# Optimization experiments

Measured on AMD Instinct MI355X. Metric: run time of the kernel, lower is better.

Reference implementation:

```python
import jax, jax.numpy as jnp
import numpy as np

T, B, D, H, O = 128, 256, 512, 1024, 1


def setup_inputs() -> dict:
    key = jax.random.key(0)
    ks = jax.random.split(key, 10)
    s_in = 1.0 / np.sqrt(D)
    s_h = 1.0 / np.sqrt(H)
    u = lambda k, shape, s: jax.random.uniform(k, shape, jnp.float32, -s, s)
    return {
        "inputs": jax.random.normal(ks[0], (T, B, D), jnp.float32),
        "hidden_state": jnp.zeros((1, B, H), jnp.float32),
        "cell_state": jnp.zeros((1, B, H), jnp.float32),
        "W1": u(ks[1], (H, D), s_in),
        "b1": u(ks[2], (H,), s_in),
        "W_ih": u(ks[3], (4 * H, H), s_h),
        "W_hh": u(ks[4], (4 * H, H), s_h),
        "b_ih": u(ks[5], (4 * H,), s_h),
        "b_hh": u(ks[6], (4 * H,), s_h),
        "W_out": u(ks[7], (O, H), s_h),
        "b_out": u(ks[8], (O,), s_h),
    }


def reference(inputs, hidden_state, cell_state, W1, b1, W_ih, W_hh, b_ih, b_hh, W_out, b_out):
    # first_layer + ReLU (dropout is identity in eval mode)
    x = jax.nn.relu(jnp.einsum("tbd,hd->tbh", inputs, W1) + b1)  # (T,B,H)
    # Precompute input contribution to all gates for every timestep.
    xg = jnp.einsum("tbh,gh->tbg", x, W_ih) + b_ih + b_hh  # (T,B,4H)
    h0 = hidden_state[0]
    c0 = cell_state[0]

    def step(carry, xg_t):
        h, c = carry
        g = xg_t + h @ W_hh.T  # (B,4H), PyTorch gate order i,f,g,o
        i, f, gg, o = jnp.split(g, 4, axis=-1)
        i = jax.nn.sigmoid(i)
        f = jax.nn.sigmoid(f)
        gg = jnp.tanh(gg)
        o = jax.nn.sigmoid(o)
        c = f * c + i * gg
        h = o * jnp.tanh(c)
        return (h, c), h

    (hT, cT), hs = jax.lax.scan(step, (h0, c0), xg)
    out = jnp.einsum("tbh,oh->tbo", hs, W_out) + b_out  # (T,B,O)
    return out, hT[None], cT[None]
```

## Files before the change

### kernel.cpp

```cpp
#include <hip/hip_runtime.h>
#include <hip/hip_bf16.h>
#include <math.h>


#define T_STEPS 128
#define BATCH   256
#define DIM     512
#define HID     1024
#define GATES   4096
#define FPAD    32

typedef __attribute__((ext_vector_type(8))) short short8;
typedef __attribute__((ext_vector_type(4))) float f4;
typedef __attribute__((ext_vector_type(4))) int i4;

__device__ __forceinline__ short f2bf(float f) {
    union { float f; unsigned u; } x; x.f = f;
    unsigned r = (x.u + 0x7fffu + ((x.u >> 16) & 1u)) >> 16;
    return (short)r;
}
__device__ __forceinline__ float bf2f(short s) {
    union { unsigned u; float f; } x; x.u = ((unsigned)(unsigned short)s) << 16;
    return x.f;
}
__device__ __forceinline__ float sigm(float x) { return 1.f / (1.f + __expf(-x)); }
__device__ __forceinline__ float tanh_fast(float x) { return 2.f / (1.f + __expf(-2.f * x)) - 1.f; }

__device__ __forceinline__ void gll16(const void* g, void* l) {
    __builtin_amdgcn_global_load_lds(
        (const __attribute__((address_space(1))) void*)g,
        (__attribute__((address_space(3))) void*)l, 16, 0, 0);
}
__device__ __forceinline__ void store16_wt(void* p, i4 v) {
    asm volatile("global_store_dwordx4 %0, %1, off sc0 sc1"
                 :: "v"(p), "v"(v) : "memory");
}

__global__ __launch_bounds__(256) void cvt_f32_bf16(const float* __restrict__ in,
                                                    short* __restrict__ out, int n4) {
    int i = blockIdx.x * 256 + threadIdx.x;
    if (i < n4) {
        float4 v = ((const float4*)in)[i];
        union { short s[4]; long long ll; } r;
        r.s[0] = f2bf(v.x); r.s[1] = f2bf(v.y); r.s[2] = f2bf(v.z); r.s[3] = f2bf(v.w);
        ((long long*)out)[i] = r.ll;
    }
}

__global__ __launch_bounds__(256) void cvt_h0_blocked(const float* __restrict__ h0,
                                                      short* __restrict__ dst) {
    int b = blockIdx.x, k0 = threadIdx.x * 4;
    float4 v = *(const float4*)&h0[(size_t)b * HID + k0];
    union { short s[4]; long long ll; } p;
    p.s[0] = f2bf(v.x); p.s[1] = f2bf(v.y); p.s[2] = f2bf(v.z); p.s[3] = f2bf(v.w);
    *(long long*)&dst[(k0 >> 3) * (BATCH * 8) + b * 8 + (k0 & 7)] = p.ll;
}

__global__ __launch_bounds__(256) void cvt_permute_rows(const float* __restrict__ in,
                                                        short* __restrict__ out) {
    int r = blockIdx.x;
    int hc = r >> 2, g = r & 3;
    const float* src = in + (size_t)(g * HID + hc) * HID;
    short* dst = out + (size_t)r * HID;
    int c = threadIdx.x * 4;
    float4 v = *(const float4*)&src[c];
    union { short s[4]; long long ll; } p;
    p.s[0] = f2bf(v.x); p.s[1] = f2bf(v.y); p.s[2] = f2bf(v.z); p.s[3] = f2bf(v.w);
    *(long long*)&dst[c] = p.ll;
}

__global__ __launch_bounds__(256) void bias_sum_perm(const float* __restrict__ a,
                                                     const float* __restrict__ b,
                                                     float* __restrict__ o) {
    int r = blockIdx.x * 256 + threadIdx.x;
    int hc = r >> 2, g = r & 3;
    int src = g * HID + hc;
    o[r] = a[src] + b[src];
}

__global__ __launch_bounds__(256) void copy_f32v4(const float* __restrict__ in,
                                                  float* __restrict__ out, int n4) {
    int i = blockIdx.x * 256 + threadIdx.x;
    if (i < n4) ((float4*)out)[i] = ((const float4*)in)[i];
}

__global__ __launch_bounds__(256) void zero_i32(int* __restrict__ p, int n) {
    for (int i = blockIdx.x * 256 + threadIdx.x; i < n; i += gridDim.x * 256)
        p[i] = 0;
}

__global__ __launch_bounds__(256) void gemm_bt2(const short* __restrict__ A,
                                                const short* __restrict__ B,
                                                const float* __restrict__ bias,
                                                short* __restrict__ C,
                                                int M, int N, int K, int do_relu) {
    __shared__ __align__(16) short As[2][128 * 64];
    __shared__ __align__(16) short Bs[2][128 * 64];
    const int tid = threadIdx.x, wave = tid >> 6, lane = tid & 63;
    const int wm = (wave >> 1) * 64, wn = (wave & 1) * 64;

    const int nwg = gridDim.x * gridDim.y;
    const int flat = blockIdx.y * gridDim.x + blockIdx.x;
    const int qq = nwg >> 3, rr = nwg & 7;
    const int xcd = flat & 7, oin = flat >> 3;
    const int swz = (xcd < rr ? xcd * (qq + 1) : rr * (qq + 1) + (xcd - rr) * qq) + oin;
    const int bm = (swz % gridDim.x) * 128, bn = (swz / gridDim.x) * 128;

#define STAGE2(bufi, kt)                                                       \
    {                                                                          \
        const int k0_ = (kt) * 64;                                             \
        _Pragma("unroll")                                                      \
        for (int u = 0; u < 4; ++u) {                                          \
            int r0 = wave * 32 + u * 8;                                        \
            int row = r0 + (lane >> 3);                                        \
            int kof = ((lane & 7) ^ (row & 7)) * 8;                            \
            gll16(&A[(size_t)(bm + row) * K + k0_ + kof], &As[bufi][r0 * 64]); \
            gll16(&B[(size_t)(bn + row) * K + k0_ + kof], &Bs[bufi][r0 * 64]); \
        }                                                                      \
    }

    f4 acc[4][4] = {};
    const int NT = K >> 6;

    STAGE2(0, 0)
    __syncthreads();

    int cur = 0;
    for (int kt = 0; kt < NT; ++kt) {
        if (kt + 1 < NT) STAGE2(cur ^ 1, kt + 1)

#pragma unroll
        for (int ks = 0; ks < 2; ++ks) {
            short8 af[4], bfr[4];
#pragma unroll
            for (int i = 0; i < 4; ++i) {
                int ra = wm + i * 16 + (lane & 15);
                int sa = (ks * 4 + (lane >> 4)) ^ (ra & 7);
                af[i] = *(const short8*)&As[cur][ra * 64 + sa * 8];
                int rb = wn + i * 16 + (lane & 15);
                int sb = (ks * 4 + (lane >> 4)) ^ (rb & 7);
                bfr[i] = *(const short8*)&Bs[cur][rb * 64 + sb * 8];
            }
            __builtin_amdgcn_s_setprio(1);
#pragma unroll
            for (int i = 0; i < 4; ++i)
#pragma unroll
                for (int j = 0; j < 4; ++j)
                    acc[i][j] = __builtin_amdgcn_mfma_f32_16x16x32_bf16(af[i], bfr[j], acc[i][j], 0, 0, 0);
            __builtin_amdgcn_s_setprio(0);
        }
        __syncthreads();
        cur ^= 1;
    }
#undef STAGE2

    const int lc = lane & 15, lr = (lane >> 4) * 4;
#pragma unroll
    for (int i = 0; i < 4; ++i) {
#pragma unroll
        for (int j = 0; j < 4; ++j) {
            int col = bn + wn + j * 16 + lc;
            float bv = bias[col];
#pragma unroll
            for (int r = 0; r < 4; ++r) {
                int row = bm + wm + i * 16 + lr + r;
                float v = acc[i][j][r] + bv;
                if (do_relu) v = fmaxf(v, 0.f);
                C[(size_t)row * N + col] = f2bf(v);
            }
        }
    }
}

__global__ __launch_bounds__(256) void lstm_persist(const short* __restrict__ Whh,
                                                    const short* __restrict__ xgc,
                                                    short* __restrict__ hist,
                                                    float* __restrict__ cf,
                                                    float* __restrict__ hT,
                                                    float* __restrict__ cT,
                                                    int* __restrict__ flags,
                                                    int* __restrict__ go,
                                                    int TC, int last) {
    __shared__ __align__(16) short Bf[32768];
    __shared__ __align__(16) short Ht[512];
    const int tid = threadIdx.x, w = tid >> 6, lane = tid & 63;
    const int bg = blockIdx.x >> 7, cg = blockIdx.x & 127;
    const int bb = bg * 64, hc0 = cg * 8;
    const int hcl = lane & 7, gp = (lane >> 3) & 1, q = lane >> 4;

#pragma unroll
    for (int i = 0; i < 16; ++i) {
        int p = w * 16 + i;
        int c = p >> 1, t = p & 1;
        gll16(&Whh[(size_t)((t * 2 + gp) * HID + hc0 + hcl) * HID + c * 32 + q * 8],
              &Bf[p * 512]);
    }

    const int rowb = bb + w * 16 + q * 4 + gp * 2;
    float creg[2];
#pragma unroll
    for (int e = 0; e < 2; ++e)
        creg[e] = cf[(size_t)(rowb + e) * HID + hc0 + hcl];

    __syncthreads();

    unsigned long long xw[2], xwn[2];
#pragma unroll
    for (int e = 0; e < 2; ++e)
        xw[e] = *(const unsigned long long*)&xgc[(size_t)(rowb + e) * GATES
                                                 + (hc0 + hcl) * 4];

#define ISSUE_A(buf, g)                                                        \
    _Pragma("unroll")                                                          \
    for (int i = 0; i < 8; ++i)                                                \
        buf[i] = *(const short8*)(abase + (size_t)((g) * 8 + i) * astr);

#define COMPUTE_A(buf, g)                                                      \
    __builtin_amdgcn_s_setprio(1);                                             \
    _Pragma("unroll")                                                          \
    for (int i = 0; i < 8; ++i) {                                              \
        short8 b0 = *(const short8*)&Bf[(((g) * 8 + i) * 2 + 0) * 512 + lane * 8]; \
        short8 b1 = *(const short8*)&Bf[(((g) * 8 + i) * 2 + 1) * 512 + lane * 8]; \
        acc0 = __builtin_amdgcn_mfma_f32_16x16x32_bf16(buf[i], b0, acc0, 0, 0, 0); \
        acc1 = __builtin_amdgcn_mfma_f32_16x16x32_bf16(buf[i], b1, acc1, 0, 0, 0); \
    }                                                                          \
    __builtin_amdgcn_s_setprio(0);

    for (int tt = 0; tt < TC; ++tt) {
        if (tt + 1 < TC) {
#pragma unroll
            for (int e = 0; e < 2; ++e)
                xwn[e] = *(const unsigned long long*)&xgc[(size_t)((tt + 1) * BATCH + rowb + e) * GATES
                                                          + (hc0 + hcl) * 4];
        }

        const short* abase = hist + (size_t)tt * BATCH * HID
                           + (size_t)q * (BATCH * 8) + (size_t)(bb + w * 16 + (lane & 15)) * 8;
        const size_t astr = (size_t)4 * (BATCH * 8);
        f4 acc0 = {}, acc1 = {};
        short8 ab0[8], ab1[8], ab2[8];
        ISSUE_A(ab0, 0)
        ISSUE_A(ab1, 1)
        ISSUE_A(ab2, 2)
        COMPUTE_A(ab0, 0)
        ISSUE_A(ab0, 3)
        COMPUTE_A(ab1, 1)
        COMPUTE_A(ab2, 2)
        COMPUTE_A(ab0, 3)

        float p0[4], p1[4];
#pragma unroll
        for (int r = 0; r < 4; ++r) {
            p0[r] = __shfl_xor(acc0[r], 8);
            p1[r] = __shfl_xor(acc1[r], 8);
        }

        int glast = last && (tt == TC - 1);
#pragma unroll
        for (int e = 0; e < 2; ++e) {
            int r = gp * 2 + e;
            size_t b = rowb + e;
            float gi = gp ? p0[r] : acc0[r];
            float gf = gp ? acc0[r] : p0[r];
            float gg = gp ? p1[r] : acc1[r];
            float go_ = gp ? acc1[r] : p1[r];
            gi += bf2f((short)(xw[e] & 0xffff));
            gf += bf2f((short)((xw[e] >> 16) & 0xffff));
            gg += bf2f((short)((xw[e] >> 32) & 0xffff));
            go_ += bf2f((short)((xw[e] >> 48) & 0xffff));
            float si = sigm(gi), sf = sigm(gf), tg = tanh_fast(gg), so = sigm(go_);
            float cn = sf * creg[e] + si * tg;
            float hv = so * tanh_fast(cn);
            creg[e] = cn;
            Ht[(w * 16 + q * 4 + gp * 2 + e) * 8 + hcl] = f2bf(hv);
            if (glast) {
                hT[b * HID + hc0 + hcl] = hv;
                cT[b * HID + hc0 + hcl] = cn;
            }
        }
        xw[0] = xwn[0]; xw[1] = xwn[1];
        __syncthreads();

        short* hn = hist + (size_t)(tt + 1) * BATCH * HID
                  + (size_t)cg * (BATCH * 8) + (size_t)bb * 8;
        if (tid < 64)
            store16_wt(&hn[tid * 8], *(const i4*)&Ht[tid * 8]);

        if (tt < TC - 1) {
            __syncthreads();
            const int base = (tt * 4 + bg) * 128 * FPAD;
            if (tid == 0)
                __hip_atomic_store(&flags[base + cg * FPAD], 1,
                                   __ATOMIC_RELAXED, __HIP_MEMORY_SCOPE_AGENT);
            if (cg == 0) {
                if (tid < 128) {
                    while (__hip_atomic_load(&flags[base + tid * FPAD],
                                             __ATOMIC_RELAXED, __HIP_MEMORY_SCOPE_AGENT) == 0)
                        __builtin_amdgcn_s_sleep(1);
                }
                __syncthreads();
                if (tid == 0)
                    __hip_atomic_store(&go[(tt * 4 + bg) * FPAD], 1,
                                       __ATOMIC_RELAXED, __HIP_MEMORY_SCOPE_AGENT);
            } else {
                if (tid == 0) {
                    while (__hip_atomic_load(&go[(tt * 4 + bg) * FPAD],
                                             __ATOMIC_RELAXED, __HIP_MEMORY_SCOPE_AGENT) == 0)
                        __builtin_amdgcn_s_sleep(1);
                }
                __syncthreads();
            }
        }
    }

#undef ISSUE_A
#undef COMPUTE_A

#pragma unroll
    for (int e = 0; e < 2; ++e)
        cf[(size_t)(rowb + e) * HID + hc0 + hcl] = creg[e];
}

__global__ __launch_bounds__(256) void out_head(const short* __restrict__ hs,
                                                const float* __restrict__ Wout,
                                                const float* __restrict__ bout,
                                                float* __restrict__ out) {
    int row = blockIdx.x * 4 + (threadIdx.x >> 6);
    int lane = threadIdx.x & 63;
    int tt = row >> 8, b = row & 255;
    const short* sb = hs + (size_t)(tt + 1) * BATCH * HID + b * 8;
    const float2* w2 = (const float2*)Wout;
    float s = 0.f;
#pragma unroll
    for (int j = 0; j < 8; ++j) {
        int m = j * 64 + lane;
        int pk = *(const int*)&sb[(size_t)(m >> 2) * (BATCH * 8) + 2 * (m & 3)];
        float2 wv = w2[m];
        union { unsigned u; float f; } lo, hi;
        lo.u = ((unsigned)pk) << 16;
        hi.u = ((unsigned)pk) & 0xffff0000u;
        s += lo.f * wv.x + hi.f * wv.y;
    }
#pragma unroll
    for (int off = 32; off; off >>= 1) s += __shfl_down(s, off);
    if (lane == 0) out[row] = s + bout[0];
}

extern "C" void kernel_launch(void* const* d_in, const int* in_sizes, int n_in,
                              void* d_out, int out_size, void* d_ws, size_t ws_size,
                              hipStream_t stream) {
    const float* inputs = (const float*)d_in[0];
    const float* h0     = (const float*)d_in[1];
    const float* c0     = (const float*)d_in[2];
    const float* W1     = (const float*)d_in[3];
    const float* b1     = (const float*)d_in[4];
    const float* W_ih   = (const float*)d_in[5];
    const float* W_hh   = (const float*)d_in[6];
    const float* b_ih   = (const float*)d_in[7];
    const float* b_hh   = (const float*)d_in[8];
    const float* W_out  = (const float*)d_in[9];
    const float* b_out  = (const float*)d_in[10];

    float* out = (float*)d_out;
    float* hT  = out + (size_t)T_STEPS * BATCH;
    float* cT  = hT + (size_t)BATCH * HID;

    char* base = (char*)d_ws;
    size_t off = 0;
    auto alloc = [&](size_t bytes) -> char* {
        char* q = base + off;
        off += (bytes + 255) & ~(size_t)255;
        return q;
    };
    short* W1b   = (short*)alloc((size_t)HID * DIM * 2);
    short* Wihb  = (short*)alloc((size_t)GATES * HID * 2);
    short* Whhb  = (short*)alloc((size_t)GATES * HID * 2);
    float* biasf = (float*)alloc((size_t)GATES * 4);
    float* cf    = (float*)alloc((size_t)BATCH * HID * 4);
    int*   flags = (int*)alloc((size_t)T_STEPS * 4 * 128 * FPAD * 4);
    int*   go    = (int*)alloc((size_t)T_STEPS * 4 * FPAD * 4);

    short* xb_a  = (short*)alloc((size_t)T_STEPS * BATCH * HID * 2);
    short* hhist = (short*)alloc((size_t)(T_STEPS + 1) * BATCH * HID * 2);

    size_t xg_all_bytes = (size_t)T_STEPS * BATCH * GATES * 2;
    size_t inb_bytes    = (size_t)T_STEPS * BATCH * DIM * 2;
    int ALLX = (ws_size - off) >= (xg_all_bytes + 4096);
    short *xgb = nullptr, *inb_a = nullptr;
    int TC = 32;
    if (ALLX) {
        xgb   = (short*)alloc(xg_all_bytes);
        inb_a = xgb;
    } else {
        size_t per_c = (size_t)TC * BATCH * GATES * 2;
        while (TC > 1 && off + (per_c > inb_bytes ? per_c : inb_bytes) + 4096 > ws_size) {
            TC >>= 1;
            per_c = (size_t)TC * BATCH * GATES * 2;
        }
        size_t region = per_c > inb_bytes ? per_c : inb_bytes;
        xgb   = (short*)alloc(region);
        inb_a = xgb;
    }

    cvt_f32_bf16<<<(HID * DIM / 4 + 255) / 256, 256, 0, stream>>>(W1, W1b, HID * DIM / 4);
    cvt_permute_rows<<<GATES, 256, 0, stream>>>(W_ih, Wihb);
    cvt_f32_bf16<<<(GATES * HID / 4 + 255) / 256, 256, 0, stream>>>(W_hh, Whhb, GATES * HID / 4);
    bias_sum_perm<<<GATES / 256, 256, 0, stream>>>(b_ih, b_hh, biasf);
    cvt_h0_blocked<<<BATCH, 256, 0, stream>>>(h0, hhist);
    copy_f32v4<<<(BATCH * HID / 4 + 255) / 256, 256, 0, stream>>>(c0, cf, BATCH * HID / 4);
    zero_i32<<<512, 256, 0, stream>>>(flags, T_STEPS * 4 * 128 * FPAD + T_STEPS * 4 * FPAD);

    {
        int Ma = T_STEPS * BATCH;
        cvt_f32_bf16<<<(Ma * DIM / 4 + 255) / 256, 256, 0, stream>>>(
            inputs, inb_a, Ma * DIM / 4);
        gemm_bt2<<<dim3(Ma / 128, HID / 128), 256, 0, stream>>>(
            inb_a, W1b, b1, xb_a, Ma, HID, DIM, 1);
        if (ALLX) {
            gemm_bt2<<<dim3(Ma / 128, GATES / 128), 256, 0, stream>>>(
                xb_a, Wihb, biasf, xgb, Ma, GATES, HID, 0);
        }
    }

    for (int t0 = 0; t0 < T_STEPS; t0 += TC) {
        int last = (t0 + TC >= T_STEPS);
        const short* xgc;
        if (ALLX) {
            xgc = xgb + (size_t)t0 * BATCH * GATES;
        } else {
            int Mc = TC * BATCH;
            gemm_bt2<<<dim3(Mc / 128, GATES / 128), 256, 0, stream>>>(
                xb_a + (size_t)t0 * BATCH * HID, Wihb, biasf, xgb,
                Mc, GATES, HID, 0);
            xgc = xgb;
        }

        lstm_persist<<<512, 256, 0, stream>>>(Whhb, xgc,
                                              hhist + (size_t)t0 * BATCH * HID,
                                              cf, hT, cT,
                                              flags + (size_t)t0 * 4 * 128 * FPAD,
                                              go + (size_t)t0 * 4 * FPAD,
                                              TC, last);
    }

    out_head<<<T_STEPS * BATCH / 4, 256, 0, stream>>>(hhist, W_out, b_out, out);
}
```

Before: 1.276 ms.

## Replace 128x128 GEMM with 256x256 eight-wave tile and interleaved staging schedule

The input-projection GEMMs now use a 256x256 block tile with 512 threads (8 waves, each computing 128x64). Global-to-LDS loads for the next k-tile are split into quarters and interleaved with the MFMA quarters, using explicit vmcnt waits and barriers in place of the old stage-then-compute loop. The larger tile raises data reuse per byte loaded and the finer interleaving is meant to hide load latency. The cost is more LDS (128KB), more accumulator registers and fewer workgroups. The tile dimensions must now divide M and N by 256.

```diff
diff --git a/kernel.cpp b/kernel.cpp
--- a/kernel.cpp
+++ b/kernel.cpp
@@ -89,82 +89,139 @@
         p[i] = 0;
 }
 
-__global__ __launch_bounds__(256) void gemm_bt2(const short* __restrict__ A,
+__global__ __launch_bounds__(512) void gemm_bt8(const short* __restrict__ A,
                                                 const short* __restrict__ B,
                                                 const float* __restrict__ bias,
                                                 short* __restrict__ C,
                                                 int M, int N, int K, int do_relu) {
-    __shared__ __align__(16) short As[2][128 * 64];
-    __shared__ __align__(16) short Bs[2][128 * 64];
-    const int tid = threadIdx.x, wave = tid >> 6, lane = tid & 63;
-    const int wm = (wave >> 1) * 64, wn = (wave & 1) * 64;
+    __shared__ __align__(16) short As[2][256 * 64];
+    __shared__ __align__(16) short Bs[2][256 * 64];
+    const int tid = threadIdx.x, w = tid >> 6, lane = tid & 63;
+    const int wr = w >> 2, wc = w & 3;
 
     const int nwg = gridDim.x * gridDim.y;
     const int flat = blockIdx.y * gridDim.x + blockIdx.x;
     const int qq = nwg >> 3, rr = nwg & 7;
     const int xcd = flat & 7, oin = flat >> 3;
     const int swz = (xcd < rr ? xcd * (qq + 1) : rr * (qq + 1) + (xcd - rr) * qq) + oin;
-    const int bm = (swz % gridDim.x) * 128, bn = (swz / gridDim.x) * 128;
-
-#define STAGE2(bufi, kt)                                                       \
-    {                                                                          \
-        const int k0_ = (kt) * 64;                                             \
+    const int bm = (swz % gridDim.x) * 256, bn = (swz / gridDim.x) * 256;
+
+    const int NT = K >> 6, NI = NT >> 1;
+
+#define STG(P, L, bmn, kt, h)                                                  \
+    if ((kt) < NT) {                                                           \
         _Pragma("unroll")                                                      \
-        for (int u = 0; u < 4; ++u) {                                          \
-            int r0 = wave * 32 + u * 8;                                        \
-            int row = r0 + (lane >> 3);                                        \
-            int kof = ((lane & 7) ^ (row & 7)) * 8;                            \
-            gll16(&A[(size_t)(bm + row) * K + k0_ + kof], &As[bufi][r0 * 64]); \
-            gll16(&B[(size_t)(bn + row) * K + k0_ + kof], &Bs[bufi][r0 * 64]); \
+        for (int s_ = 0; s_ < 2; ++s_) {                                       \
+            int r0_ = (h) * 128 + s_ * 64 + w * 8;                             \
+            int row_ = r0_ + (lane >> 3);                                      \
+            int kof_ = ((lane & 7) ^ (row_ & 7)) * 8;                          \
+            gll16(&P[(size_t)((bmn) + row_) * K + (kt) * 64 + kof_],           \
+                  &L[(kt) & 1][r0_ * 64]);                                     \
         }                                                                      \
     }
 
-    f4 acc[4][4] = {};
-    const int NT = K >> 6;
-
-    STAGE2(0, 0)
-    __syncthreads();
-
-    int cur = 0;
-    for (int kt = 0; kt < NT; ++kt) {
-        if (kt + 1 < NT) STAGE2(cur ^ 1, kt + 1)
-
-#pragma unroll
-        for (int ks = 0; ks < 2; ++ks) {
-            short8 af[4], bfr[4];
-#pragma unroll
-            for (int i = 0; i < 4; ++i) {
-                int ra = wm + i * 16 + (lane & 15);
-                int sa = (ks * 4 + (lane >> 4)) ^ (ra & 7);
-                af[i] = *(const short8*)&As[cur][ra * 64 + sa * 8];
-                int rb = wn + i * 16 + (lane & 15);
-                int sb = (ks * 4 + (lane >> 4)) ^ (rb & 7);
-                bfr[i] = *(const short8*)&Bs[cur][rb * 64 + sb * 8];
-            }
-            __builtin_amdgcn_s_setprio(1);
-#pragma unroll
-            for (int i = 0; i < 4; ++i)
-#pragma unroll
-                for (int j = 0; j < 4; ++j)
-                    acc[i][j] = __builtin_amdgcn_mfma_f32_16x16x32_bf16(af[i], bfr[j], acc[i][j], 0, 0, 0);
-            __builtin_amdgcn_s_setprio(0);
-        }
-        __syncthreads();
-        cur ^= 1;
-    }
-#undef STAGE2
+#define LOADB(kt)                                                              \
+    _Pragma("unroll")                                                          \
+    for (int nf = 0; nf < 4; ++nf)                                             \
+        _Pragma("unroll")                                                      \
+        for (int ks = 0; ks < 2; ++ks) {                                       \
+            int rb_ = wc * 64 + nf * 16 + (lane & 15);                         \
+            int sb_ = (ks * 4 + (lane >> 4)) ^ (rb_ & 7);                      \
+            bfr[nf][ks] = *(const short8*)&Bs[(kt) & 1][rb_ * 64 + sb_ * 8];   \
+        }
+
+#define LOADA(kt, q)                                                           \
+    _Pragma("unroll")                                                          \
+    for (int mi = 0; mi < 2; ++mi)                                             \
+        _Pragma("unroll")                                                      \
+        for (int ks = 0; ks < 2; ++ks) {                                       \
+            int ra_ = wr * 128 + ((q) * 2 + mi) * 16 + (lane & 15);            \
+            int sa_ = (ks * 4 + (lane >> 4)) ^ (ra_ & 7);                      \
+            af[mi][ks] = *(const short8*)&As[(kt) & 1][ra_ * 64 + sa_ * 8];    \
+        }
+
+#define MFMAQ(q)                                                               \
+    __builtin_amdgcn_s_setprio(1);                                             \
+    _Pragma("unroll")                                                          \
+    for (int mi = 0; mi < 2; ++mi)                                             \
+        _Pragma("unroll")                                                      \
+        for (int nf = 0; nf < 4; ++nf)                                         \
+            _Pragma("unroll")                                                  \
+            for (int ks = 0; ks < 2; ++ks)                                     \
+                acc[(q) * 2 + mi][nf] = __builtin_amdgcn_mfma_f32_16x16x32_bf16( \
+                    af[mi][ks], bfr[nf][ks], acc[(q) * 2 + mi][nf], 0, 0, 0);  \
+    __builtin_amdgcn_s_setprio(0);                                             \
+    __builtin_amdgcn_sched_barrier(0);
+
+#define VM4 asm volatile("s_waitcnt vmcnt(4)" ::: "memory");
+#define VM0 asm volatile("s_waitcnt vmcnt(0)" ::: "memory");
+#define BAR __builtin_amdgcn_s_barrier();
+
+    f4 acc[8][4] = {};
+
+    STG(A, As, bm, 0, 0) STG(A, As, bm, 0, 1)
+    STG(B, Bs, bn, 0, 0) STG(B, Bs, bn, 0, 1)
+    STG(B, Bs, bn, 1, 0) STG(B, Bs, bn, 1, 1)
+
+    for (int it = 0; it < NI; ++it) {
+        const int kt0 = 2 * it, kt1 = 2 * it + 1;
+        const int lastit = (it + 1 == NI);
+        short8 bfr[4][2], af[2][2];
+
+        VM4 BAR
+        LOADB(kt0) LOADA(kt0, 0)
+        STG(A, As, bm, kt1, 0)
+        MFMAQ(0)
+        BAR
+        LOADA(kt0, 1)
+        STG(A, As, bm, kt1, 1)
+        MFMAQ(1)
+        BAR
+        LOADA(kt0, 2)
+        STG(B, Bs, bn, kt0 + 2, 0)
+        MFMAQ(2)
+        BAR
+        LOADA(kt0, 3)
+        STG(B, Bs, bn, kt0 + 2, 1)
+        MFMAQ(3)
+
+        if (lastit) { VM0 } else { VM4 }
+        BAR
+        LOADB(kt1) LOADA(kt1, 0)
+        STG(A, As, bm, kt0 + 2, 0)
+        MFMAQ(0)
+        BAR
+        LOADA(kt1, 1)
+        STG(A, As, bm, kt0 + 2, 1)
+        MFMAQ(1)
+        BAR
+        LOADA(kt1, 2)
+        STG(B, Bs, bn, kt1 + 2, 0)
+        MFMAQ(2)
+        BAR
+        LOADA(kt1, 3)
+        STG(B, Bs, bn, kt1 + 2, 1)
+        MFMAQ(3)
+    }
+#undef STG
+#undef LOADB
+#undef LOADA
+#undef MFMAQ
+#undef VM4
+#undef VM0
+#undef BAR
 
     const int lc = lane & 15, lr = (lane >> 4) * 4;
 #pragma unroll
-    for (int i = 0; i < 4; ++i) {
-#pragma unroll
-        for (int j = 0; j < 4; ++j) {
-            int col = bn + wn + j * 16 + lc;
+    for (int mf = 0; mf < 8; ++mf) {
+#pragma unroll
+        for (int nf = 0; nf < 4; ++nf) {
+            int col = bn + wc * 64 + nf * 16 + lc;
             float bv = bias[col];
 #pragma unroll
             for (int r = 0; r < 4; ++r) {
-                int row = bm + wm + i * 16 + lr + r;
-                float v = acc[i][j][r] + bv;
+                int row = bm + wr * 128 + mf * 16 + lr + r;
+                float v = acc[mf][nf][r] + bv;
                 if (do_relu) v = fmaxf(v, 0.f);
                 C[(size_t)row * N + col] = f2bf(v);
             }
@@ -414,10 +471,10 @@
         int Ma = T_STEPS * BATCH;
         cvt_f32_bf16<<<(Ma * DIM / 4 + 255) / 256, 256, 0, stream>>>(
             inputs, inb_a, Ma * DIM / 4);
-        gemm_bt2<<<dim3(Ma / 128, HID / 128), 256, 0, stream>>>(
+        gemm_bt8<<<dim3(Ma / 256, HID / 256), 512, 0, stream>>>(
             inb_a, W1b, b1, xb_a, Ma, HID, DIM, 1);
         if (ALLX) {
-            gemm_bt2<<<dim3(Ma / 128, GATES / 128), 256, 0, stream>>>(
+            gemm_bt8<<<dim3(Ma / 256, GATES / 256), 512, 0, stream>>>(
                 xb_a, Wihb, biasf, xgb, Ma, GATES, HID, 0);
         }
     }
@@ -429,7 +486,7 @@
             xgc = xgb + (size_t)t0 * BATCH * GATES;
         } else {
             int Mc = TC * BATCH;
-            gemm_bt2<<<dim3(Mc / 128, GATES / 128), 256, 0, stream>>>(
+            gemm_bt8<<<dim3(Mc / 256, GATES / 256), 512, 0, stream>>>(
                 xb_a + (size_t)t0 * BATCH * HID, Wihb, biasf, xgb,
                 Mc, GATES, HID, 0);
             xgc = xgb;
```

Result: faster. 1.166 ms (-8.6%).
